# Performance work log

Measured on AMD Instinct MI355X. Metric: run time of the kernel, lower is better.

The kernel has to match this reference:

```python
import jax, jax.numpy as jnp
import numpy as np

B, P = 4, 50000
D_IN, COND = 3, 48
# layer l: in IN_DIMS[l] -> out OUT_DIMS[l]; dims=[3,256*8,257], skip at layer index 4
IN_DIMS  = [D_IN + COND, 256, 256, 256, 256, 256, 256, 256, 256]
OUT_DIMS = [256, 256, 256, 253, 256, 256, 256, 256, 257]
N_LIN = 9
INV_SQRT2 = np.float32(1.0 / np.sqrt(2.0))


def softplus_beta100(x):
    return jax.nn.softplus(100.0 * x) * 0.01


def setup_inputs() -> dict:
    key = jax.random.key(0)
    ks = jax.random.split(key, 2 + 2 * N_LIN)
    inp = {
        "input": jax.random.normal(ks[0], (B, P, D_IN), dtype=jnp.float32),
        "cond_pose": jax.random.normal(ks[1], (B, COND), dtype=jnp.float32),
    }
    for l in range(N_LIN):
        scale = np.float32(np.sqrt(2.0 / OUT_DIMS[l]))  # geometry-style init scale
        inp[f"W{l}"] = jax.random.normal(ks[2 + 2 * l], (OUT_DIMS[l], IN_DIMS[l]), dtype=jnp.float32) * scale
        inp[f"b{l}"] = jnp.zeros((OUT_DIMS[l],), dtype=jnp.float32)
    return inp


def reference(input, cond_pose,
              W0, b0, W1, b1, W2, b2, W3, b3, W4, b4, W5, b5, W6, b6, W7, b7, W8, b8):
    Ws = [W0, W1, W2, W3, W4, W5, W6, W7, W8]
    bs = [b0, b1, b2, b3, b4, b5, b6, b7, b8]
    nb, npnt, nd = input.shape
    x_in = input.reshape(nb * npnt, nd)                                   # (N, 3)
    c = jnp.broadcast_to(cond_pose[:, None, :], (nb, npnt, COND)).reshape(nb * npnt, COND)
    x = jnp.concatenate([x_in, c], axis=-1)                               # cond concat at layer 0
    for l in range(N_LIN):
        if l == 4:  # skip connection: concat raw input, scaled by 1/sqrt(2)
            x = jnp.concatenate([x, x_in], axis=-1) * INV_SQRT2
        x = x @ Ws[l].T + bs[l]
        if l < N_LIN - 1:
            x = softplus_beta100(x)
    return x.reshape(nb, npnt, -1)                                        # (B, P, 257)
```

## Files before the change

kernel.cpp:

```cpp
#include <hip/hip_runtime.h>


typedef __attribute__((ext_vector_type(8))) short bf16x8;
typedef __attribute__((ext_vector_type(4))) float f32x4;
typedef __attribute__((ext_vector_type(2))) float f32x2;

#define PPTS 50000

__device__ __forceinline__ short f2bf(float f) {
    union { float f; unsigned u; } v; v.f = f;
    unsigned r = v.u + 0x7fffu + ((v.u >> 16) & 1u);
    return (short)(r >> 16);
}

__device__ __forceinline__ unsigned cvt_pk_bf16(float lo, float hi) {
    unsigned r;
    asm("v_cvt_pk_bf16_f32 %0, %1, %2" : "=v"(r) : "v"(lo), "v"(hi));
    return r;
}

__device__ __forceinline__ void bar_lgkm() {
    asm volatile("s_waitcnt lgkmcnt(0)" ::: "memory");
    __builtin_amdgcn_s_barrier();
    __builtin_amdgcn_sched_barrier(0);
}

__device__ __forceinline__ f32x2 sp100_pair(f32x2 y) {
    const f32x2 A2 = {6.9314718e-3f, 6.9314718e-3f};
    const f32x2 B2 = {-3.11522e-3f, -3.11522e-3f};
    const f32x2 C2 = {9.8829e-4f,  9.8829e-4f};
    const f32x2 K2 = {-144.26950408889634f, -144.26950408889634f};
    const f32x2 Z2 = {0.0f, 0.0f};
    f32x2 m = __builtin_elementwise_abs(y) * K2;
    f32x2 e = {__builtin_amdgcn_exp2f(m.x), __builtin_amdgcn_exp2f(m.y)};
    f32x2 t = __builtin_elementwise_fma(C2, e, B2);
    t = __builtin_elementwise_fma(t, e, A2);
    return __builtin_elementwise_fma(e, t, __builtin_elementwise_max(y, Z2));
}
__device__ __forceinline__ void sp100_4(f32x4& v) {
    f32x2 y0 = {v[0], v[1]}, y1 = {v[2], v[3]};
    f32x2 r0 = sp100_pair(y0), r1 = sp100_pair(y1);
    v[0] = r0.x; v[1] = r0.y; v[2] = r1.x; v[3] = r1.y;
}

__device__ __forceinline__ int xswz(int row) {
    return (((row & 7) ^ (5 * ((row >> 3) & 1))) << 4);
}
__device__ __forceinline__ short* xaddr(short* base, int row, int col) {
    int off = ((row << 9) + (col << 1)) ^ xswz(row);
    return (short*)((char*)base + off);
}
__device__ __forceinline__ const short* xaddrc(const short* base, int row, int col) {
    int off = ((row << 9) + (col << 1)) ^ xswz(row);
    return (const short*)((const char*)base + off);
}

__global__ void prep_kernel(
    const float* __restrict__ W0, const float* __restrict__ W1, const float* __restrict__ W2,
    const float* __restrict__ W3, const float* __restrict__ W4, const float* __restrict__ W5,
    const float* __restrict__ W6, const float* __restrict__ W7, const float* __restrict__ W8,
    short* __restrict__ wbf)
{
    const int gid = blockIdx.x * blockDim.x + threadIdx.x;
    if (gid >= 68096) return;
    int l, cid; const float* Wsrc;
    if      (gid <  2048) { l = 0; cid = gid;         Wsrc = W0; }
    else if (gid < 10240) { l = 1; cid = gid -  2048; Wsrc = W1; }
    else if (gid < 18432) { l = 2; cid = gid - 10240; Wsrc = W2; }
    else if (gid < 26624) { l = 3; cid = gid - 18432; Wsrc = W3; }
    else if (gid < 34816) { l = 4; cid = gid - 26624; Wsrc = W4; }
    else if (gid < 43008) { l = 5; cid = gid - 34816; Wsrc = W5; }
    else if (gid < 51200) { l = 6; cid = gid - 43008; Wsrc = W6; }
    else if (gid < 59392) { l = 7; cid = gid - 51200; Wsrc = W7; }
    else                  { l = 8; cid = gid - 59392; Wsrc = W8; }
    const int NR   = (l == 3) ? 253 : ((l == 8) ? 257 : 256);
    const int KR   = (l == 0) ? 51 : 256;
    const int klog = (l == 0) ? 1 : 3;
    const float sc = (l == 4) ? 0.70710678f : 1.0f;
    const int lane  = cid & 63;
    const int tile  = cid >> 6;
    const int ntile = tile >> klog;
    const int ktile = tile & ((1 << klog) - 1);
    const int n  = ntile * 16 + (lane & 15);
    const int k0 = ktile * 32 + ((lane >> 4) << 3);
    bf16x8 v;
#pragma unroll
    for (int j = 0; j < 8; ++j) {
        int k = k0 + j;
        float f = (n < NR && k < KR) ? Wsrc[n * KR + k] * sc : 0.0f;
        v[j] = f2bf(f);
    }
    ((bf16x8*)wbf)[gid] = v;
}

template<int KSTEPS, int MODE>
__device__ __forceinline__ void layer_fwd(short* xb,
    const bf16x8* __restrict__ wl, const bf16x8* __restrict__ wlnext,
    const float* __restrict__ bias, int lane, int wid, bf16x8 (&ap)[4])
{
    const int prow = lane & 15;
    const int kg   = (lane >> 4) << 3;
    const int rb4  = (lane >> 4) << 2;
    f32x4 acc[4][4];
#pragma unroll
    for (int nii = 0; nii < 4; ++nii) {
        const int cb = (wid * 4 + nii) * 16 + rb4;
        f32x4 bv;
        if (MODE == 1 && cb == 252) { f32x4 tb = {bias[252], 0.f, 0.f, 0.f}; bv = tb; }
        else bv = *(const f32x4*)(bias + cb);
#pragma unroll
        for (int mi = 0; mi < 4; ++mi)
            acc[mi][nii] = bv;
    }
    bf16x8 a_cur[4], b_cur[4];
#pragma unroll
    for (int nii = 0; nii < 4; ++nii) a_cur[nii] = ap[nii];
#pragma unroll
    for (int mi = 0; mi < 4; ++mi)
        b_cur[mi] = *(const bf16x8*)xaddrc(xb, mi * 16 + prow, kg);
#pragma unroll
    for (int ks = 0; ks < KSTEPS; ++ks) {
        bf16x8 a_nxt[4], b_nxt[4];
        if (ks + 1 < KSTEPS) {
#pragma unroll
            for (int nii = 0; nii < 4; ++nii)
                a_nxt[nii] = wl[((wid * 4 + nii) * KSTEPS + ks + 1) * 64 + lane];
#pragma unroll
            for (int mi = 0; mi < 4; ++mi)
                b_nxt[mi] = *(const bf16x8*)xaddrc(xb, mi * 16 + prow,
                                                   (ks + 1) * 32 + kg);
        } else {
#pragma unroll
            for (int nii = 0; nii < 4; ++nii)
                a_nxt[nii] = wlnext[(wid * 4 + nii) * 512 + lane];
        }
        __builtin_amdgcn_s_setprio(1);
#pragma unroll
        for (int mi = 0; mi < 4; ++mi)
#pragma unroll
            for (int nii = 0; nii < 4; ++nii)
                acc[mi][nii] = __builtin_amdgcn_mfma_f32_16x16x32_bf16(
                    a_cur[nii], b_cur[mi], acc[mi][nii], 0, 0, 0);
        __builtin_amdgcn_s_setprio(0);
#pragma unroll
        for (int nii = 0; nii < 4; ++nii) a_cur[nii] = a_nxt[nii];
        if (ks + 1 < KSTEPS) {
#pragma unroll
            for (int mi = 0; mi < 4; ++mi) b_cur[mi] = b_nxt[mi];
        }
    }
#pragma unroll
    for (int nii = 0; nii < 4; ++nii) ap[nii] = a_cur[nii];
#pragma unroll
    for (int nii = 0; nii < 4; ++nii)
#pragma unroll
        for (int mi = 0; mi < 4; ++mi)
            sp100_4(acc[mi][nii]);
    bar_lgkm();
#pragma unroll
    for (int nii = 0; nii < 4; ++nii) {
        const int cb = (wid * 4 + nii) * 16 + rb4;
#pragma unroll
        for (int mi = 0; mi < 4; ++mi) {
            unsigned p01 = cvt_pk_bf16(acc[mi][nii][0], acc[mi][nii][1]);
            unsigned p23 = cvt_pk_bf16(acc[mi][nii][2], acc[mi][nii][3]);
            if (MODE == 1 && cb == 252) {
                *xaddr(xb, mi * 16 + prow, 252) = (short)(p01 & 0xffff);
            } else {
                uint2 pk; pk.x = p01; pk.y = p23;
                *(uint2*)xaddr(xb, mi * 16 + prow, cb) = pk;
            }
        }
    }
}

__global__ __launch_bounds__(256, 2) void net_kernel(
    const float* __restrict__ xin, const float* __restrict__ cond,
    const bf16x8* __restrict__ W,
    const float* __restrict__ b0, const float* __restrict__ b1, const float* __restrict__ b2,
    const float* __restrict__ b3, const float* __restrict__ b4, const float* __restrict__ b5,
    const float* __restrict__ b6, const float* __restrict__ b7, const float* __restrict__ b8,
    float* __restrict__ out)
{
    __shared__ short xb[64 * 256];
    const int t    = threadIdx.x;
    const int pt0  = blockIdx.x * 64;
    const int lane = t & 63;
    const int wid  = t >> 6;

    bf16x8 ap[4];
#pragma unroll
    for (int nii = 0; nii < 4; ++nii)
        ap[nii] = W[(wid * 4 + nii) * 128 + lane];

    float sk[3] = {0.f, 0.f, 0.f};
    if (t < 64) {
#pragma unroll
        for (int c = 0; c < 3; ++c)
            sk[c] = xin[(pt0 + t) * 3 + c];
    }

    {
        const int row   = t >> 2;
        const int c0    = (t & 3) << 4;
        const int point = pt0 + row;
        const int batch = point / PPTS;
        const float* xp = xin + point * 3;
        const float* cp = cond + batch * 48;
#pragma unroll
        for (int h = 0; h < 2; ++h) {
            bf16x8 v;
#pragma unroll
            for (int i = 0; i < 8; ++i) {
                int c = c0 + h * 8 + i;
                float f = (c < 3) ? xp[c] : ((c < 51) ? cp[c - 3] : 0.0f);
                v[i] = f2bf(f);
            }
            *(bf16x8*)xaddr(xb, row, c0 + h * 8) = v;
        }
    }
    bar_lgkm();

    layer_fwd<2, 0>(xb, W +     0, W +  2048, b0, lane, wid, ap); bar_lgkm();
    layer_fwd<8, 0>(xb, W +  2048, W + 10240, b1, lane, wid, ap); bar_lgkm();
    layer_fwd<8, 0>(xb, W + 10240, W + 18432, b2, lane, wid, ap); bar_lgkm();
    layer_fwd<8, 1>(xb, W + 18432, W + 26624, b3, lane, wid, ap);
    if (t < 64) {
#pragma unroll
        for (int c = 0; c < 3; ++c)
            *xaddr(xb, t, 253 + c) = f2bf(sk[c]);
    }
    bar_lgkm();
    layer_fwd<8, 0>(xb, W + 26624, W + 34816, b4, lane, wid, ap); bar_lgkm();
    layer_fwd<8, 0>(xb, W + 34816, W + 43008, b5, lane, wid, ap); bar_lgkm();
    layer_fwd<8, 0>(xb, W + 43008, W + 51200, b6, lane, wid, ap); bar_lgkm();
    layer_fwd<8, 0>(xb, W + 51200, W + 59392, b7, lane, wid, ap); bar_lgkm();

    {
        const bf16x8* wl = W + 59392;
        const int prow = lane & 15;
        const int kg   = (lane >> 4) << 3;
        const int rb4  = (lane >> 4) << 2;
        const float blast = b8[256];
#pragma unroll
        for (int half = 0; half < 2; ++half) {
            f32x4 acc[2][4];
            f32x4 acc2[2];
#pragma unroll
            for (int nii = 0; nii < 4; ++nii) {
                const int cb = (wid * 4 + nii) * 16 + rb4;
                const f32x4 bv = *(const f32x4*)(b8 + cb);
#pragma unroll
                for (int m2 = 0; m2 < 2; ++m2)
                    acc[m2][nii] = bv;
            }
            {
                f32x4 bz = {(rb4 == 0) ? blast : 0.f, 0.f, 0.f, 0.f};
                acc2[0] = bz; acc2[1] = bz;
            }
            bf16x8 a_cur[4], b_cur[2];
#pragma unroll
            for (int nii = 0; nii < 4; ++nii)
                a_cur[nii] = (half == 0) ? ap[nii]
                           : wl[((wid * 4 + nii) * 8) * 64 + lane];
#pragma unroll
            for (int m2 = 0; m2 < 2; ++m2)
                b_cur[m2] = *(const bf16x8*)xaddrc(xb, (half * 2 + m2) * 16 + prow, kg);
#pragma unroll
            for (int ks = 0; ks < 8; ++ks) {
                bf16x8 a_nxt[4], b_nxt[2], a2;
                if (ks < 7) {
#pragma unroll
                    for (int nii = 0; nii < 4; ++nii)
                        a_nxt[nii] = wl[((wid * 4 + nii) * 8 + ks + 1) * 64 + lane];
#pragma unroll
                    for (int m2 = 0; m2 < 2; ++m2)
                        b_nxt[m2] = *(const bf16x8*)xaddrc(xb, (half * 2 + m2) * 16 + prow,
                                                           (ks + 1) * 32 + kg);
                }
                if (wid == 0) a2 = wl[(128 + ks) * 64 + lane];
                __builtin_amdgcn_s_setprio(1);
#pragma unroll
                for (int m2 = 0; m2 < 2; ++m2)
#pragma unroll
                    for (int nii = 0; nii < 4; ++nii)
                        acc[m2][nii] = __builtin_amdgcn_mfma_f32_16x16x32_bf16(
                            a_cur[nii], b_cur[m2], acc[m2][nii], 0, 0, 0);
                if (wid == 0) {
#pragma unroll
                    for (int m2 = 0; m2 < 2; ++m2)
                        acc2[m2] = __builtin_amdgcn_mfma_f32_16x16x32_bf16(
                            a2, b_cur[m2], acc2[m2], 0, 0, 0);
                }
                __builtin_amdgcn_s_setprio(0);
                if (ks < 7) {
#pragma unroll
                    for (int nii = 0; nii < 4; ++nii) a_cur[nii] = a_nxt[nii];
#pragma unroll
                    for (int m2 = 0; m2 < 2; ++m2)  b_cur[m2]  = b_nxt[m2];
                }
            }
#pragma unroll
            for (int nii = 0; nii < 4; ++nii) {
                const int cb = (wid * 4 + nii) * 16 + rb4;
#pragma unroll
                for (int m2 = 0; m2 < 2; ++m2) {
                    const int rowoff = (pt0 + (half * 2 + m2) * 16 + prow) * 257 + cb;
#pragma unroll
                    for (int r = 0; r < 4; ++r)
                        out[rowoff + r] = acc[m2][nii][r];
                }
            }
            if (wid == 0 && rb4 == 0) {
#pragma unroll
                for (int m2 = 0; m2 < 2; ++m2)
                    out[(pt0 + (half * 2 + m2) * 16 + prow) * 257 + 256]
                        = acc2[m2][0];
            }
        }
    }
}

extern "C" void kernel_launch(void* const* d_in, const int* in_sizes, int n_in,
                              void* d_out, int out_size, void* d_ws, size_t ws_size,
                              hipStream_t stream)
{
    const float* xin  = (const float*)d_in[0];
    const float* cond = (const float*)d_in[1];
    const float* Wp[9]; const float* bp[9];
    for (int l = 0; l < 9; ++l) { Wp[l] = (const float*)d_in[2 + 2 * l]; bp[l] = (const float*)d_in[3 + 2 * l]; }
    short* wbf = (short*)d_ws;

    prep_kernel<<<dim3(266), dim3(256), 0, stream>>>(
        Wp[0], Wp[1], Wp[2], Wp[3], Wp[4], Wp[5], Wp[6], Wp[7], Wp[8], wbf);
    net_kernel<<<dim3(3125), dim3(256), 0, stream>>>(
        xin, cond, (const bf16x8*)wbf,
        bp[0], bp[1], bp[2], bp[3], bp[4], bp[5], bp[6], bp[7], bp[8],
        (float*)d_out);
}
```

Measured before the change: 282.1 us.

## Double-buffer activation LDS to drop one barrier per layer and prefetch biases

Activations now ping-pong between two shared-memory buffers, so each layer reads from one buffer and writes to the other. This removes the barrier that separated the softplus epilogue from the LDS writes. Next-layer biases are loaded during the current layer's epilogue and carried in registers. The final layer now loads its B operand from LDS inside each k-step instead of software-prefetching it. Shared memory per block doubles to 64KB, which may limit occupancy at two blocks per CU.

```diff
diff --git a/kernel.cpp b/kernel.cpp
--- a/kernel.cpp
+++ b/kernel.cpp
@@ -93,31 +93,27 @@
     ((bf16x8*)wbf)[gid] = v;
 }
 
-template<int KSTEPS, int MODE>
-__device__ __forceinline__ void layer_fwd(short* xb,
+template<int KSTEPS, int MODE, int MODE_NEXT>
+__device__ __forceinline__ void layer_fwd(const short* src, short* dst,
     const bf16x8* __restrict__ wl, const bf16x8* __restrict__ wlnext,
-    const float* __restrict__ bias, int lane, int wid, bf16x8 (&ap)[4])
+    const float* __restrict__ bias_next, int lane, int wid,
+    bf16x8 (&ap)[4], f32x4 (&bp)[4])
 {
     const int prow = lane & 15;
     const int kg   = (lane >> 4) << 3;
     const int rb4  = (lane >> 4) << 2;
     f32x4 acc[4][4];
 #pragma unroll
-    for (int nii = 0; nii < 4; ++nii) {
-        const int cb = (wid * 4 + nii) * 16 + rb4;
-        f32x4 bv;
-        if (MODE == 1 && cb == 252) { f32x4 tb = {bias[252], 0.f, 0.f, 0.f}; bv = tb; }
-        else bv = *(const f32x4*)(bias + cb);
+    for (int nii = 0; nii < 4; ++nii)
 #pragma unroll
         for (int mi = 0; mi < 4; ++mi)
-            acc[mi][nii] = bv;
-    }
+            acc[mi][nii] = bp[nii];
     bf16x8 a_cur[4], b_cur[4];
 #pragma unroll
     for (int nii = 0; nii < 4; ++nii) a_cur[nii] = ap[nii];
 #pragma unroll
     for (int mi = 0; mi < 4; ++mi)
-        b_cur[mi] = *(const bf16x8*)xaddrc(xb, mi * 16 + prow, kg);
+        b_cur[mi] = *(const bf16x8*)xaddrc(src, mi * 16 + prow, kg);
 #pragma unroll
     for (int ks = 0; ks < KSTEPS; ++ks) {
         bf16x8 a_nxt[4], b_nxt[4];
@@ -127,7 +123,7 @@
                 a_nxt[nii] = wl[((wid * 4 + nii) * KSTEPS + ks + 1) * 64 + lane];
 #pragma unroll
             for (int mi = 0; mi < 4; ++mi)
-                b_nxt[mi] = *(const bf16x8*)xaddrc(xb, mi * 16 + prow,
+                b_nxt[mi] = *(const bf16x8*)xaddrc(src, mi * 16 + prow,
                                                    (ks + 1) * 32 + kg);
         } else {
 #pragma unroll
@@ -152,11 +148,19 @@
 #pragma unroll
     for (int nii = 0; nii < 4; ++nii) ap[nii] = a_cur[nii];
 #pragma unroll
+    for (int nii = 0; nii < 4; ++nii) {
+        const int cb = (wid * 4 + nii) * 16 + rb4;
+        if (MODE_NEXT == 1 && cb == 252) {
+            f32x4 tb = {bias_next[252], 0.f, 0.f, 0.f}; bp[nii] = tb;
+        } else {
+            bp[nii] = *(const f32x4*)(bias_next + cb);
+        }
+    }
+#pragma unroll
     for (int nii = 0; nii < 4; ++nii)
 #pragma unroll
         for (int mi = 0; mi < 4; ++mi)
             sp100_4(acc[mi][nii]);
-    bar_lgkm();
 #pragma unroll
     for (int nii = 0; nii < 4; ++nii) {
         const int cb = (wid * 4 + nii) * 16 + rb4;
@@ -165,10 +169,10 @@
             unsigned p01 = cvt_pk_bf16(acc[mi][nii][0], acc[mi][nii][1]);
             unsigned p23 = cvt_pk_bf16(acc[mi][nii][2], acc[mi][nii][3]);
             if (MODE == 1 && cb == 252) {
-                *xaddr(xb, mi * 16 + prow, 252) = (short)(p01 & 0xffff);
+                *xaddr(dst, mi * 16 + prow, 252) = (short)(p01 & 0xffff);
             } else {
                 uint2 pk; pk.x = p01; pk.y = p23;
-                *(uint2*)xaddr(xb, mi * 16 + prow, cb) = pk;
+                *(uint2*)xaddr(dst, mi * 16 + prow, cb) = pk;
             }
         }
     }
@@ -182,16 +186,21 @@
     const float* __restrict__ b6, const float* __restrict__ b7, const float* __restrict__ b8,
     float* __restrict__ out)
 {
-    __shared__ short xb[64 * 256];
+    __shared__ short xb0[64 * 256];
+    __shared__ short xb1[64 * 256];
     const int t    = threadIdx.x;
     const int pt0  = blockIdx.x * 64;
     const int lane = t & 63;
     const int wid  = t >> 6;
+    const int rb4  = (lane >> 4) << 2;
 
     bf16x8 ap[4];
-#pragma unroll
-    for (int nii = 0; nii < 4; ++nii)
+    f32x4  bp[4];
+#pragma unroll
+    for (int nii = 0; nii < 4; ++nii) {
         ap[nii] = W[(wid * 4 + nii) * 128 + lane];
+        bp[nii] = *(const f32x4*)(b0 + (wid * 4 + nii) * 16 + rb4);
+    }
 
     float sk[3] = {0.f, 0.f, 0.f};
     if (t < 64) {
@@ -216,31 +225,29 @@
                 float f = (c < 3) ? xp[c] : ((c < 51) ? cp[c - 3] : 0.0f);
                 v[i] = f2bf(f);
             }
-            *(bf16x8*)xaddr(xb, row, c0 + h * 8) = v;
+            *(bf16x8*)xaddr(xb0, row, c0 + h * 8) = v;
         }
     }
     bar_lgkm();
 
-    layer_fwd<2, 0>(xb, W +     0, W +  2048, b0, lane, wid, ap); bar_lgkm();
-    layer_fwd<8, 0>(xb, W +  2048, W + 10240, b1, lane, wid, ap); bar_lgkm();
-    layer_fwd<8, 0>(xb, W + 10240, W + 18432, b2, lane, wid, ap); bar_lgkm();
-    layer_fwd<8, 1>(xb, W + 18432, W + 26624, b3, lane, wid, ap);
+    layer_fwd<2, 0, 0>(xb0, xb1, W +     0, W +  2048, b1, lane, wid, ap, bp); bar_lgkm();
+    layer_fwd<8, 0, 0>(xb1, xb0, W +  2048, W + 10240, b2, lane, wid, ap, bp); bar_lgkm();
+    layer_fwd<8, 0, 1>(xb0, xb1, W + 10240, W + 18432, b3, lane, wid, ap, bp); bar_lgkm();
     if (t < 64) {
 #pragma unroll
         for (int c = 0; c < 3; ++c)
-            *xaddr(xb, t, 253 + c) = f2bf(sk[c]);
-    }
-    bar_lgkm();
-    layer_fwd<8, 0>(xb, W + 26624, W + 34816, b4, lane, wid, ap); bar_lgkm();
-    layer_fwd<8, 0>(xb, W + 34816, W + 43008, b5, lane, wid, ap); bar_lgkm();
-    layer_fwd<8, 0>(xb, W + 43008, W + 51200, b6, lane, wid, ap); bar_lgkm();
-    layer_fwd<8, 0>(xb, W + 51200, W + 59392, b7, lane, wid, ap); bar_lgkm();
+            *xaddr(xb0, t, 253 + c) = f2bf(sk[c]);
+    }
+    layer_fwd<8, 1, 0>(xb1, xb0, W + 18432, W + 26624, b4, lane, wid, ap, bp); bar_lgkm();
+    layer_fwd<8, 0, 0>(xb0, xb1, W + 26624, W + 34816, b5, lane, wid, ap, bp); bar_lgkm();
+    layer_fwd<8, 0, 0>(xb1, xb0, W + 34816, W + 43008, b6, lane, wid, ap, bp); bar_lgkm();
+    layer_fwd<8, 0, 0>(xb0, xb1, W + 43008, W + 51200, b7, lane, wid, ap, bp); bar_lgkm();
+    layer_fwd<8, 0, 0>(xb1, xb0, W + 51200, W + 59392, b8, lane, wid, ap, bp); bar_lgkm();
 
     {
         const bf16x8* wl = W + 59392;
         const int prow = lane & 15;
         const int kg   = (lane >> 4) << 3;
-        const int rb4  = (lane >> 4) << 2;
         const float blast = b8[256];
 #pragma unroll
         for (int half = 0; half < 2; ++half) {
@@ -248,56 +255,50 @@
             f32x4 acc2[2];
 #pragma unroll
             for (int nii = 0; nii < 4; ++nii) {
-                const int cb = (wid * 4 + nii) * 16 + rb4;
-                const f32x4 bv = *(const f32x4*)(b8 + cb);
 #pragma unroll
                 for (int m2 = 0; m2 < 2; ++m2)
-                    acc[m2][nii] = bv;
+                    acc[m2][nii] = bp[nii];
             }
             {
                 f32x4 bz = {(rb4 == 0) ? blast : 0.f, 0.f, 0.f, 0.f};
                 acc2[0] = bz; acc2[1] = bz;
             }
-            bf16x8 a_cur[4], b_cur[2];
+            bf16x8 a_cur[4];
 #pragma unroll
             for (int nii = 0; nii < 4; ++nii)
                 a_cur[nii] = (half == 0) ? ap[nii]
                            : wl[((wid * 4 + nii) * 8) * 64 + lane];
 #pragma unroll
-            for (int m2 = 0; m2 < 2; ++m2)
-                b_cur[m2] = *(const bf16x8*)xaddrc(xb, (half * 2 + m2) * 16 + prow, kg);
-#pragma unroll
             for (int ks = 0; ks < 8; ++ks) {
-                bf16x8 a_nxt[4], b_nxt[2], a2;
+                bf16x8 a_nxt[4], a2;
                 if (ks < 7) {
 #pragma unroll
                     for (int nii = 0; nii < 4; ++nii)
                         a_nxt[nii] = wl[((wid * 4 + nii) * 8 + ks + 1) * 64 + lane];
-#pragma unroll
-                    for (int m2 = 0; m2 < 2; ++m2)
-                        b_nxt[m2] = *(const bf16x8*)xaddrc(xb, (half * 2 + m2) * 16 + prow,
-                                                           (ks + 1) * 32 + kg);
                 }
                 if (wid == 0) a2 = wl[(128 + ks) * 64 + lane];
+                bf16x8 b[2];
+#pragma unroll
+                for (int m2 = 0; m2 < 2; ++m2)
+                    b[m2] = *(const bf16x8*)xaddrc(xb0, (half * 2 + m2) * 16 + prow,
+                                                   ks * 32 + kg);
                 __builtin_amdgcn_s_setprio(1);
 #pragma unroll
                 for (int m2 = 0; m2 < 2; ++m2)
 #pragma unroll
                     for (int nii = 0; nii < 4; ++nii)
                         acc[m2][nii] = __builtin_amdgcn_mfma_f32_16x16x32_bf16(
-                            a_cur[nii], b_cur[m2], acc[m2][nii], 0, 0, 0);
+                            a_cur[nii], b[m2], acc[m2][nii], 0, 0, 0);
                 if (wid == 0) {
 #pragma unroll
                     for (int m2 = 0; m2 < 2; ++m2)
                         acc2[m2] = __builtin_amdgcn_mfma_f32_16x16x32_bf16(
-                            a2, b_cur[m2], acc2[m2], 0, 0, 0);
+                            a2, b[m2], acc2[m2], 0, 0, 0);
                 }
                 __builtin_amdgcn_s_setprio(0);
                 if (ks < 7) {
 #pragma unroll
                     for (int nii = 0; nii < 4; ++nii) a_cur[nii] = a_nxt[nii];
-#pragma unroll
-                    for (int m2 = 0; m2 < 2; ++m2)  b_cur[m2]  = b_nxt[m2];
                 }
             }
 #pragma unroll
```

New measurement: 279.5 us (median of 2 runs). About the same (-0.9%).
